# Optimization experiments

Measured on AMD Instinct MI355X. Metric: run time of the kernel, lower is better.

The kernel has to match this reference:

```python
import jax, jax.numpy as jnp
import numpy as np

B, L, D, H = 2, 2048, 512, 8
HD = D // H  # head_dim used only for the concat/reshape trick


def setup_inputs() -> dict:
    key = jax.random.key(0)
    ks = jax.random.split(key, 7)
    s = 0.02  # small init so softmax isn't saturated
    return {
        "q": jax.random.normal(ks[0], (B, L, D), jnp.float32),
        "k": jax.random.normal(ks[1], (B, L, D), jnp.float32),
        "v": jax.random.normal(ks[2], (B, L, D), jnp.float32),
        # per-head full-width projections: W[h] is the nn.Linear weight [out,in]
        "Wq": jax.random.normal(ks[3], (H, D, D), jnp.float32) * s,
        "Wk": jax.random.normal(ks[4], (H, D, D), jnp.float32) * s,
        "Wv": jax.random.normal(ks[5], (H, D, D), jnp.float32) * s,
        # output_layer Linear(d_model*num_heads -> d_model, bias=False)
        "Wo": jax.random.normal(ks[6], (D, H * D), jnp.float32) * s,
    }


def reference(q, k, v, Wq, Wk, Wv, Wo):
    # Each head applies its own full d_model x d_model projections (Linear: x @ W^T)
    qh = jnp.einsum('bld,hed->bhle', q, Wq)  # [B,H,L,D]
    kh = jnp.einsum('bld,hed->bhle', k, Wk)
    vh = jnp.einsum('bld,hed->bhle', v, Wv)
    # scaled by sqrt(d_k) with d_k = d_model (as in the original code)
    scores = jnp.einsum('bhle,bhme->bhlm', qh, kh) / jnp.sqrt(jnp.float32(D))
    attn = jax.nn.softmax(scores, axis=-1)          # [B,H,L,L] (dropout = identity in eval)
    ctx = jnp.einsum('bhlm,bhme->bhle', attn, vh)   # [B,H,L,D]
    # torch: each head ctx [B,L,D] -> view(B,L,H,HD); cat over heads on last dim -> [B,L,H,H*HD]; flatten
    comb = ctx.reshape(B, H, L, H, HD).transpose(0, 2, 3, 1, 4).reshape(B, L, H * D)
    out = comb @ Wo.T                               # [B,L,D]
    return out, attn
```

## Files before the change

### kernel.cpp

```cpp
#include <hip/hip_runtime.h>
#include <cstdio>
#include <cstdint>


#define AS1 __attribute__((address_space(1)))
#define AS3 __attribute__((address_space(3)))

typedef __attribute__((ext_vector_type(8))) short bf16x8;
typedef __attribute__((ext_vector_type(4))) short short4v;
typedef __attribute__((ext_vector_type(4))) float f32x4;

constexpr int cB = 2, cH = 8, cL = 2048, cD = 512;
constexpr float SCORE_SCALE = 0.044194173824159216f;

__device__ __forceinline__ short f2bf(float f) {
  return __builtin_bit_cast(short, static_cast<__bf16>(f));
}

__device__ __forceinline__ void gload16(const void* g, void* l) {
  __builtin_amdgcn_global_load_lds((AS1 const void*)g, (AS3 void*)l, 16, 0, 0);
}

struct CvtArgs { const float4* s[7]; short4v* d[7]; };

__global__ __launch_bounds__(256) void cvt_all(CvtArgs a) {
  const int z = blockIdx.y;
  const int i = blockIdx.x * 256 + threadIdx.x;
  const float4 v = a.s[z][i];
  short4v o = { f2bf(v.x), f2bf(v.y), f2bf(v.z), f2bf(v.w) };
  a.d[z][i] = o;
}

enum { M_PROJ = 0, M_PROJV = 1, M_SCORES = 2, M_OUT = 3 };

template <int MODE>
__global__ __launch_bounds__(256) void gemm_nt(const short* __restrict__ Ap,
                                               const short* __restrict__ Bp,
                                               void* __restrict__ Cp,
                                               float2* __restrict__ Sp) {
  constexpr int K   = (MODE == M_OUT) ? 1024 : 512;
  constexpr int LDA = (MODE == M_OUT) ? 4096 : 512;
  constexpr int LDB = (MODE == M_OUT) ? 4096 : 512;

  __shared__ short As[3][128 * 32];
  __shared__ short Bs[3][128 * 32];

  const int t = threadIdx.x;
  const int lane = t & 63;
  const int wv = t >> 6;
  const int wm = wv >> 1, wn = wv & 1;
  const int z = blockIdx.z;

  size_t Aoff, Boff;
  if constexpr (MODE == M_PROJ || MODE == M_PROJV) {
    Aoff = (size_t)(z >> 3) * ((size_t)cL * cD);
    Boff = (size_t)(z & 7) * ((size_t)cD * cD);
  } else if constexpr (MODE == M_SCORES) {
    Aoff = (size_t)z * ((size_t)cL * cD);
    Boff = (size_t)z * ((size_t)cL * cD);
  } else {
    Aoff = (size_t)(z >> 2) * ((size_t)cL * 4096) + (size_t)(z & 3) * 1024;
    Boff = (size_t)(z & 3) * 1024;
  }

  const short* Ag0 = Ap + Aoff + (size_t)(blockIdx.y * 128) * LDA;
  const short* Bg0 = Bp + Boff + (size_t)(blockIdx.x * 128) * LDB;

  f32x4 acc[4][4];
#pragma unroll
  for (int i = 0; i < 4; ++i)
#pragma unroll
    for (int j = 0; j < 4; ++j) acc[i][j] = (f32x4){0.f, 0.f, 0.f, 0.f};

  auto stage = [&](int b, int kt) {
#pragma unroll
    for (int r = 0; r < 2; ++r) {
      const int cbase = r * 256 + wv * 64;
      const int c = cbase + lane;
      const int row = c >> 2, col = (c & 3) * 8;
      gload16(Ag0 + (size_t)row * LDA + kt + col, &As[b][cbase * 8]);
    }
#pragma unroll
    for (int r = 0; r < 2; ++r) {
      const int cbase = r * 256 + wv * 64;
      const int c = cbase + lane;
      const int row = c >> 2, col = (c & 3) * 8;
      gload16(Bg0 + (size_t)row * LDB + kt + col, &Bs[b][cbase * 8]);
    }
  };

  const int koff = (lane >> 4) * 8;
  const int ar = wm * 64 + (lane & 15);
  const int br = wn * 64 + (lane & 15);

  constexpr int nt = K / 32;
  stage(0, 0);
  stage(1, 32);
  int cur = 0, pre = 2;
  for (int tt = 0; tt < nt; ++tt) {
    if (tt < nt - 1) { asm volatile("s_waitcnt vmcnt(4) lgkmcnt(0)" ::: "memory"); }
    else             { asm volatile("s_waitcnt vmcnt(0) lgkmcnt(0)" ::: "memory"); }
    __builtin_amdgcn_sched_barrier(0);
    __builtin_amdgcn_s_barrier();
    __builtin_amdgcn_sched_barrier(0);
    if (tt + 2 < nt) stage(pre, (tt + 2) * 32);
    __builtin_amdgcn_sched_barrier(0);

    bf16x8 af[4], bfv[4];
#pragma unroll
    for (int i = 0; i < 4; ++i) af[i] = *(const bf16x8*)&As[cur][(ar + i * 16) * 32 + koff];
#pragma unroll
    for (int j = 0; j < 4; ++j) bfv[j] = *(const bf16x8*)&Bs[cur][(br + j * 16) * 32 + koff];
    __builtin_amdgcn_s_setprio(1);
#pragma unroll
    for (int i = 0; i < 4; ++i)
#pragma unroll
      for (int j = 0; j < 4; ++j)
        acc[i][j] = __builtin_amdgcn_mfma_f32_16x16x32_bf16(af[i], bfv[j], acc[i][j], 0, 0, 0);
    __builtin_amdgcn_s_setprio(0);
    cur = (cur == 2) ? 0 : cur + 1;
    pre = (pre == 2) ? 0 : pre + 1;
  }

  const int r0 = (lane >> 4) * 4;
  const int cc = lane & 15;
  const int rowbase = blockIdx.y * 128 + wm * 64 + r0;
  const int colbase = blockIdx.x * 128 + wn * 64 + cc;

  if constexpr (MODE == M_PROJ) {
    short* C = (short*)Cp + (size_t)z * ((size_t)cL * cD);
#pragma unroll
    for (int i = 0; i < 4; ++i)
#pragma unroll
      for (int j = 0; j < 4; ++j)
#pragma unroll
        for (int r = 0; r < 4; ++r)
          C[(size_t)(rowbase + i * 16 + r) * cD + (colbase + j * 16)] = f2bf(acc[i][j][r]);
  } else if constexpr (MODE == M_PROJV) {
    short* C = (short*)Cp + (size_t)z * ((size_t)cD * cL);
#pragma unroll
    for (int i = 0; i < 4; ++i)
#pragma unroll
      for (int j = 0; j < 4; ++j) {
        short4v o = { f2bf(acc[i][j][0]), f2bf(acc[i][j][1]),
                      f2bf(acc[i][j][2]), f2bf(acc[i][j][3]) };
        *(short4v*)&C[(size_t)(colbase + j * 16) * cL + (rowbase + i * 16)] = o;
      }
  } else if constexpr (MODE == M_SCORES) {
    float* C = (float*)Cp + (size_t)z * ((size_t)cL * cL);
    float2* ps = Sp + (size_t)z * ((size_t)cL * 32);
    const int pid = blockIdx.x * 2 + wn;
#pragma unroll
    for (int i = 0; i < 4; ++i) {
      float sv[4][4];
#pragma unroll
      for (int j = 0; j < 4; ++j)
#pragma unroll
        for (int r = 0; r < 4; ++r) sv[j][r] = acc[i][j][r] * SCORE_SCALE;
#pragma unroll
      for (int j = 0; j < 4; ++j)
#pragma unroll
        for (int r = 0; r < 4; ++r)
          C[(size_t)(rowbase + i * 16 + r) * cL + (colbase + j * 16)] = sv[j][r];
#pragma unroll
      for (int r = 0; r < 4; ++r) {
        float mx = fmaxf(fmaxf(sv[0][r], sv[1][r]), fmaxf(sv[2][r], sv[3][r]));
#pragma unroll
        for (int off = 1; off < 16; off <<= 1) mx = fmaxf(mx, __shfl_xor(mx, off, 64));
        float sm = __expf(sv[0][r] - mx) + __expf(sv[1][r] - mx) +
                   __expf(sv[2][r] - mx) + __expf(sv[3][r] - mx);
#pragma unroll
        for (int off = 1; off < 16; off <<= 1) sm += __shfl_xor(sm, off, 64);
        if ((lane & 15) == 0)
          ps[(size_t)(rowbase + i * 16 + r) * 32 + pid] = make_float2(mx, sm);
      }
    }
  } else {
    float* C = (float*)Cp + (size_t)((z & 3) * 2 + (z >> 2)) * ((size_t)cL * cD);
#pragma unroll
    for (int i = 0; i < 4; ++i)
#pragma unroll
      for (int j = 0; j < 4; ++j)
#pragma unroll
        for (int r = 0; r < 4; ++r)
          C[(size_t)(rowbase + i * 16 + r) * cD + (colbase + j * 16)] = acc[i][j][r];
  }
}

__global__ __launch_bounds__(256) void combine_stats(const float2* __restrict__ ps,
                                                     float2* __restrict__ stats) {
  const int row = blockIdx.x * 256 + threadIdx.x;
  const float2* p = ps + (size_t)row * 32;
  float m = -1e30f;
#pragma unroll
  for (int i = 0; i < 32; ++i) m = fmaxf(m, p[i].x);
  float l = 0.f;
#pragma unroll
  for (int i = 0; i < 32; ++i) l += p[i].y * __expf(p[i].x - m);
  stats[row] = make_float2(m, 1.0f / l);
}

__global__ __launch_bounds__(512, 4) void fused_ctx(const short* __restrict__ vhT,
                                                    const float2* __restrict__ stats,
                                                    float* __restrict__ attn,
                                                    short* __restrict__ comb) {
  __shared__ short Bs[2][512 * 32];
  __shared__ short Pb[2][64 * 32];

  const int t = threadIdx.x;
  const int lane = t & 63;
  const int wv = t >> 6;
  const int rowblk = blockIdx.x;
  const int z = blockIdx.y;

  const int trow = t >> 3;
  const int tcb = t & 7;
  const int pidx = trow * 32 + (((tcb >> 1) ^ ((trow >> 1) & 3)) << 3) + ((tcb & 1) << 2);
  const int grow = rowblk * 64 + trow;
  float* sp = attn + ((size_t)z * cL + grow) * cL + tcb * 4;
  const float2 st = stats[(size_t)z * cL + grow];
  const float m = st.x, invl = st.y;

  const short* Bg = vhT + (size_t)z * ((size_t)cD * cL);

  f32x4 acc[4][4];
#pragma unroll
  for (int i = 0; i < 4; ++i)
#pragma unroll
    for (int j = 0; j < 4; ++j) acc[i][j] = (f32x4){0.f, 0.f, 0.f, 0.f};

  const int qk = lane >> 4;
  const int arr = lane & 15;
  const int br = wv * 64 + (lane & 15);

  auto stageB = [&](int nb, int kt) {
#pragma unroll
    for (int r = 0; r < 4; ++r) {
      const int cbase = r * 512 + wv * 64;
      const int c = cbase + lane;
      const int row = c >> 2;
      const int swcol = ((c & 3) ^ ((row >> 1) & 3)) * 8;
      gload16(Bg + (size_t)row * cL + kt + swcol, &Bs[nb][cbase * 8]);
    }
  };
  auto transform = [&](int ck, float4 v) -> short4v {
    float* dst = sp + ck * 32;
    const float p0 = __expf(v.x - m) * invl;
    const float p1 = __expf(v.y - m) * invl;
    const float p2 = __expf(v.z - m) * invl;
    const float p3 = __expf(v.w - m) * invl;
    *(float4*)dst = make_float4(p0, p1, p2, p3);
    short4v pb = { f2bf(p0), f2bf(p1), f2bf(p2), f2bf(p3) };
    return pb;
  };

  stageB(0, 0);
  float4 c = *(const float4*)(sp);
  short4v pb = transform(0, c);
  c = *(const float4*)(sp + 32);
  *(short4v*)&Pb[0][pidx] = pb;

  for (int k = 0; k < 63; ++k) {
    const int cb = k & 1, nb = cb ^ 1;
    pb = transform(k + 1, c);
    const int kc = (k + 2) & 63;
    c = *(const float4*)(sp + kc * 32);
    asm volatile("s_waitcnt vmcnt(2) lgkmcnt(0)" ::: "memory");
    __builtin_amdgcn_sched_barrier(0);
    __builtin_amdgcn_s_barrier();
    __builtin_amdgcn_sched_barrier(0);
    *(short4v*)&Pb[nb][pidx] = pb;
    stageB(nb, (k + 1) * 32);
    __builtin_amdgcn_sched_barrier(0);
    bf16x8 af[4], bfv[4];
#pragma unroll
    for (int i = 0; i < 4; ++i) {
      const int rA = arr + i * 16;
      af[i] = *(const bf16x8*)&Pb[cb][rA * 32 + ((qk ^ ((rA >> 1) & 3)) << 3)];
    }
#pragma unroll
    for (int j = 0; j < 4; ++j) {
      const int rB = br + j * 16;
      bfv[j] = *(const bf16x8*)&Bs[cb][rB * 32 + ((qk ^ ((rB >> 1) & 3)) << 3)];
    }
    __builtin_amdgcn_s_setprio(1);
#pragma unroll
    for (int i = 0; i < 4; ++i)
#pragma unroll
      for (int j = 0; j < 4; ++j)
        acc[i][j] = __builtin_amdgcn_mfma_f32_16x16x32_bf16(af[i], bfv[j], acc[i][j], 0, 0, 0);
    __builtin_amdgcn_s_setprio(0);
  }

  asm volatile("s_waitcnt vmcnt(0) lgkmcnt(0)" ::: "memory");
  __builtin_amdgcn_sched_barrier(0);
  __builtin_amdgcn_s_barrier();
  __builtin_amdgcn_sched_barrier(0);
  {
    bf16x8 af[4], bfv[4];
#pragma unroll
    for (int i = 0; i < 4; ++i) {
      const int rA = arr + i * 16;
      af[i] = *(const bf16x8*)&Pb[1][rA * 32 + ((qk ^ ((rA >> 1) & 3)) << 3)];
    }
#pragma unroll
    for (int j = 0; j < 4; ++j) {
      const int rB = br + j * 16;
      bfv[j] = *(const bf16x8*)&Bs[1][rB * 32 + ((qk ^ ((rB >> 1) & 3)) << 3)];
    }
    __builtin_amdgcn_s_setprio(1);
#pragma unroll
    for (int i = 0; i < 4; ++i)
#pragma unroll
      for (int j = 0; j < 4; ++j)
        acc[i][j] = __builtin_amdgcn_mfma_f32_16x16x32_bf16(af[i], bfv[j], acc[i][j], 0, 0, 0);
    __builtin_amdgcn_s_setprio(0);
  }

  const int r0 = (lane >> 4) * 4;
  const int cc = lane & 15;
  short* C = comb + (size_t)(z >> 3) * ((size_t)cL * (cH * cD));
  const int h = z & 7;
  const int rowbase = rowblk * 64 + r0;
#pragma unroll
  for (int i = 0; i < 4; ++i)
#pragma unroll
    for (int j = 0; j < 4; ++j) {
      const int e = wv * 64 + j * 16 + cc;
      const int jc = ((e >> 6) << 9) + (h << 6) + (e & 63);
#pragma unroll
      for (int r = 0; r < 4; ++r)
        C[(size_t)(rowbase + i * 16 + r) * (cH * cD) + jc] = f2bf(acc[i][j][r]);
    }
}

__global__ __launch_bounds__(256) void add_quads(const float4* __restrict__ p,
                                                 float4* __restrict__ out) {
  const int i = blockIdx.x * 256 + threadIdx.x;
  constexpr int S = (cB * cL * cD) / 4;
  const float4 a = p[i], b = p[i + S], c = p[i + 2 * S], d = p[i + 3 * S];
  out[i] = make_float4(a.x + b.x + c.x + d.x, a.y + b.y + c.y + d.y,
                       a.z + b.z + c.z + d.z, a.w + b.w + c.w + d.w);
}

extern "C" void kernel_launch(void* const* d_in, const int* in_sizes, int n_in,
                              void* d_out, int out_size, void* d_ws, size_t ws_size,
                              hipStream_t stream) {
  (void)in_sizes; (void)n_in; (void)out_size;

  const float* q  = (const float*)d_in[0];
  const float* k  = (const float*)d_in[1];
  const float* v  = (const float*)d_in[2];
  const float* Wq = (const float*)d_in[3];
  const float* Wk = (const float*)d_in[4];
  const float* Wv = (const float*)d_in[5];
  const float* Wo = (const float*)d_in[6];

  float* out  = (float*)d_out;
  float* attn = out + (size_t)cB * cL * cD;

  constexpr size_t Mi = 1ull << 20;
  char* ws = (char*)d_ws;
  short* qbf = (short*)(ws + 0 * Mi);
  short* kbf = (short*)(ws + 4 * Mi);
  short* vbf = (short*)(ws + 8 * Mi);
  short* wqb = (short*)(ws + 12 * Mi);
  short* wkb = (short*)(ws + 16 * Mi);
  short* wvb = (short*)(ws + 20 * Mi);
  short* wob = (short*)(ws + 24 * Mi);
  short* qh  = (short*)(ws + 28 * Mi);
  short* kh  = (short*)(ws + 60 * Mi);
  short* vhT = (short*)(ws + 92 * Mi);
  short* comb = qh;
  float2* stats  = (float2*)(ws + 0 * Mi);
  float2* pstats = (float2*)(ws + 4 * Mi);
  float*  pout   = (float*)(ws + 60 * Mi);

  if (ws_size < 124 * Mi) {
    fprintf(stderr, "kernel_launch: ws too small (%zu < %zu)\n", ws_size, 124 * Mi);
    return;
  }

  CvtArgs ca;
  ca.s[0] = (const float4*)q;  ca.d[0] = (short4v*)qbf;
  ca.s[1] = (const float4*)k;  ca.d[1] = (short4v*)kbf;
  ca.s[2] = (const float4*)v;  ca.d[2] = (short4v*)vbf;
  ca.s[3] = (const float4*)Wq; ca.d[3] = (short4v*)wqb;
  ca.s[4] = (const float4*)Wk; ca.d[4] = (short4v*)wkb;
  ca.s[5] = (const float4*)Wv; ca.d[5] = (short4v*)wvb;
  ca.s[6] = (const float4*)Wo; ca.d[6] = (short4v*)wob;
  cvt_all<<<dim3(2048, 7), 256, 0, stream>>>(ca);

  gemm_nt<M_PROJ ><<<dim3(4, 16, 16), 256, 0, stream>>>(qbf, wqb, qh, nullptr);
  gemm_nt<M_PROJ ><<<dim3(4, 16, 16), 256, 0, stream>>>(kbf, wkb, kh, nullptr);
  gemm_nt<M_PROJV><<<dim3(4, 16, 16), 256, 0, stream>>>(vbf, wvb, vhT, nullptr);

  gemm_nt<M_SCORES><<<dim3(16, 16, 16), 256, 0, stream>>>(qh, kh, attn, pstats);

  combine_stats<<<cB * cH * cL / 256, 256, 0, stream>>>(pstats, stats);

  fused_ctx<<<dim3(32, cB * cH), 512, 0, stream>>>(vhT, stats, attn, comb);

  gemm_nt<M_OUT><<<dim3(4, 16, 8), 256, 0, stream>>>(comb, wob, (void*)pout, nullptr);

  add_quads<<<2048, 256, 0, stream>>>((const float4*)pout, (float4*)out);
}
```

Before: 740.5 us.

## Store scores as fp16 in attn row tail, fold stats combine into ctx kernel

```diff
diff --git a/kernel.cpp b/kernel.cpp
--- a/kernel.cpp
+++ b/kernel.cpp
@@ -9,6 +9,7 @@
 typedef __attribute__((ext_vector_type(8))) short bf16x8;
 typedef __attribute__((ext_vector_type(4))) short short4v;
 typedef __attribute__((ext_vector_type(4))) float f32x4;
+typedef __attribute__((ext_vector_type(4))) _Float16 h4;
 
 constexpr int cB = 2, cH = 8, cL = 2048, cD = 512;
 constexpr float SCORE_SCALE = 0.044194173824159216f;
@@ -147,7 +148,7 @@
         *(short4v*)&C[(size_t)(colbase + j * 16) * cL + (rowbase + i * 16)] = o;
       }
   } else if constexpr (MODE == M_SCORES) {
-    float* C = (float*)Cp + (size_t)z * ((size_t)cL * cL);
+    char* Cb = (char*)Cp + ((size_t)z << 24);
     float2* ps = Sp + (size_t)z * ((size_t)cL * 32);
     const int pid = blockIdx.x * 2 + wn;
 #pragma unroll
@@ -160,8 +161,13 @@
 #pragma unroll
       for (int j = 0; j < 4; ++j)
 #pragma unroll
-        for (int r = 0; r < 4; ++r)
-          C[(size_t)(rowbase + i * 16 + r) * cL + (colbase + j * 16)] = sv[j][r];
+        for (int r = 0; r < 4; ++r) {
+          const _Float16 hv = (_Float16)sv[j][r];
+          __builtin_nontemporal_store(
+              __builtin_bit_cast(short, hv),
+              (short*)(Cb + (size_t)(rowbase + i * 16 + r) * 8192 + 4096 +
+                       (size_t)(colbase + j * 16) * 2));
+        }
 #pragma unroll
       for (int r = 0; r < 4; ++r) {
         float mx = fmaxf(fmaxf(sv[0][r], sv[1][r]), fmaxf(sv[2][r], sv[3][r]));
@@ -187,21 +193,8 @@
   }
 }
 
-__global__ __launch_bounds__(256) void combine_stats(const float2* __restrict__ ps,
-                                                     float2* __restrict__ stats) {
-  const int row = blockIdx.x * 256 + threadIdx.x;
-  const float2* p = ps + (size_t)row * 32;
-  float m = -1e30f;
-#pragma unroll
-  for (int i = 0; i < 32; ++i) m = fmaxf(m, p[i].x);
-  float l = 0.f;
-#pragma unroll
-  for (int i = 0; i < 32; ++i) l += p[i].y * __expf(p[i].x - m);
-  stats[row] = make_float2(m, 1.0f / l);
-}
-
 __global__ __launch_bounds__(512, 4) void fused_ctx(const short* __restrict__ vhT,
-                                                    const float2* __restrict__ stats,
+                                                    const float2* __restrict__ pstats,
                                                     float* __restrict__ attn,
                                                     short* __restrict__ comb) {
   __shared__ short Bs[2][512 * 32];
@@ -217,9 +210,21 @@
   const int tcb = t & 7;
   const int pidx = trow * 32 + (((tcb >> 1) ^ ((trow >> 1) & 3)) << 3) + ((tcb & 1) << 2);
   const int grow = rowblk * 64 + trow;
-  float* sp = attn + ((size_t)z * cL + grow) * cL + tcb * 4;
-  const float2 st = stats[(size_t)z * cL + grow];
-  const float m = st.x, invl = st.y;
+
+  const float2* pp = pstats + ((size_t)z * cL + grow) * 32 + tcb * 4;
+  const float2 q0 = pp[0], q1 = pp[1], q2 = pp[2], q3 = pp[3];
+  float m = fmaxf(fmaxf(q0.x, q1.x), fmaxf(q2.x, q3.x));
+#pragma unroll
+  for (int off = 1; off < 8; off <<= 1) m = fmaxf(m, __shfl_xor(m, off, 64));
+  float l = q0.y * __expf(q0.x - m) + q1.y * __expf(q1.x - m) +
+            q2.y * __expf(q2.x - m) + q3.y * __expf(q3.x - m);
+#pragma unroll
+  for (int off = 1; off < 8; off <<= 1) l += __shfl_xor(l, off, 64);
+  const float invl = 1.0f / l;
+
+  char* rowb = (char*)attn + ((size_t)z << 24) + (size_t)grow * 8192;
+  float* spf = (float*)rowb + tcb * 4;
+  const h4* sph = (const h4*)(rowb + 4096);
 
   const short* Bg = vhT + (size_t)z * ((size_t)cD * cL);
 
@@ -243,28 +248,27 @@
       gload16(Bg + (size_t)row * cL + kt + swcol, &Bs[nb][cbase * 8]);
     }
   };
-  auto transform = [&](int ck, float4 v) -> short4v {
-    float* dst = sp + ck * 32;
-    const float p0 = __expf(v.x - m) * invl;
-    const float p1 = __expf(v.y - m) * invl;
-    const float p2 = __expf(v.z - m) * invl;
-    const float p3 = __expf(v.w - m) * invl;
-    *(float4*)dst = make_float4(p0, p1, p2, p3);
+  auto transform = [&](int ck, h4 hv) -> short4v {
+    const float p0 = __expf((float)hv[0] - m) * invl;
+    const float p1 = __expf((float)hv[1] - m) * invl;
+    const float p2 = __expf((float)hv[2] - m) * invl;
+    const float p3 = __expf((float)hv[3] - m) * invl;
+    __builtin_nontemporal_store((f32x4){p0, p1, p2, p3}, (f32x4*)(spf + ck * 32));
     short4v pb = { f2bf(p0), f2bf(p1), f2bf(p2), f2bf(p3) };
     return pb;
   };
 
   stageB(0, 0);
-  float4 c = *(const float4*)(sp);
-  short4v pb = transform(0, c);
-  c = *(const float4*)(sp + 32);
+  h4 hc = __builtin_nontemporal_load(sph + tcb);
+  short4v pb = transform(0, hc);
+  hc = __builtin_nontemporal_load(sph + tcb + 8);
   *(short4v*)&Pb[0][pidx] = pb;
 
   for (int k = 0; k < 63; ++k) {
     const int cb = k & 1, nb = cb ^ 1;
-    pb = transform(k + 1, c);
+    pb = transform(k + 1, hc);
     const int kc = (k + 2) & 63;
-    c = *(const float4*)(sp + kc * 32);
+    hc = __builtin_nontemporal_load(sph + tcb + kc * 8);
     asm volatile("s_waitcnt vmcnt(2) lgkmcnt(0)" ::: "memory");
     __builtin_amdgcn_sched_barrier(0);
     __builtin_amdgcn_s_barrier();
@@ -334,13 +338,16 @@
     }
 }
 
-__global__ __launch_bounds__(256) void add_quads(const float4* __restrict__ p,
-                                                 float4* __restrict__ out) {
+__global__ __launch_bounds__(256) void add_quads(const float* __restrict__ p,
+                                                 float* __restrict__ out) {
   const int i = blockIdx.x * 256 + threadIdx.x;
-  constexpr int S = (cB * cL * cD) / 4;
-  const float4 a = p[i], b = p[i + S], c = p[i + 2 * S], d = p[i + 3 * S];
-  out[i] = make_float4(a.x + b.x + c.x + d.x, a.y + b.y + c.y + d.y,
-                       a.z + b.z + c.z + d.z, a.w + b.w + c.w + d.w);
+  constexpr int S = cB * cL * cD;
+  const f32x4 a = __builtin_nontemporal_load((const f32x4*)p + i);
+  const f32x4 b = __builtin_nontemporal_load((const f32x4*)(p + S) + i);
+  const f32x4 c = __builtin_nontemporal_load((const f32x4*)(p + 2 * S) + i);
+  const f32x4 d = __builtin_nontemporal_load((const f32x4*)(p + 3 * S) + i);
+  const f32x4 s = a + b + c + d;
+  *((f32x4*)out + i) = s;
 }
 
 extern "C" void kernel_launch(void* const* d_in, const int* in_sizes, int n_in,
@@ -372,7 +379,6 @@
   short* kh  = (short*)(ws + 60 * Mi);
   short* vhT = (short*)(ws + 92 * Mi);
   short* comb = qh;
-  float2* stats  = (float2*)(ws + 0 * Mi);
   float2* pstats = (float2*)(ws + 4 * Mi);
   float*  pout   = (float*)(ws + 60 * Mi);
 
@@ -397,11 +403,9 @@
 
   gemm_nt<M_SCORES><<<dim3(16, 16, 16), 256, 0, stream>>>(qh, kh, attn, pstats);
 
-  combine_stats<<<cB * cH * cL / 256, 256, 0, stream>>>(pstats, stats);
-
-  fused_ctx<<<dim3(32, cB * cH), 512, 0, stream>>>(vhT, stats, attn, comb);
+  fused_ctx<<<dim3(32, cB * cH), 512, 0, stream>>>(vhT, pstats, attn, comb);
 
   gemm_nt<M_OUT><<<dim3(4, 16, 8), 256, 0, stream>>>(comb, wob, (void*)pout, nullptr);
 
-  add_quads<<<2048, 256, 0, stream>>>((const float4*)pout, (float4*)out);
-}
+  add_quads<<<2048, 256, 0, stream>>>(pout, out);
+}
```

Measured after the change: 709.6 us. -4.2%, faster.
